# Optimization experiments

Measured on AMD Instinct MI355X. Metric: run time of the kernel, lower is better.

Reference implementation:

```python
import jax, jax.numpy as jnp
import numpy as np

GAMMA = 2
EPS = 1e-8  # torch F.cosine_similarity norm clamp


def setup_inputs() -> dict:
    key = jax.random.key(0)
    k1, k2, k3 = jax.random.split(key, 3)
    b, c, h, w = 32, 256, 32, 32
    x = jax.random.normal(k1, (b, c, h, w), dtype=jnp.float32)
    # 1x1 conv transform_net (num_layers=1): weight (c_out, c_in), bias (c_out,)
    conv_w = jax.random.normal(k2, (c, c), dtype=jnp.float32) / np.sqrt(c)
    conv_b = jax.random.normal(k3, (c,), dtype=jnp.float32) * 0.01
    return {"x": x, "conv_w": conv_w, "conv_b": conv_b}


def reference(x, conv_w, conv_b):
    b, c, h, w = x.shape
    hw = h * w
    xf = x.reshape(b, c, hw)  # (b, c, hw)
    # cosine similarity: normalize channels once, then a single GEMM
    norm = jnp.sqrt(jnp.sum(xf * xf, axis=1, keepdims=True))
    xn = xf / jnp.maximum(norm, EPS)
    sim = jnp.einsum('bcq,bck->bqk', xn, xn)  # (b, hw, hw)
    sim = jax.nn.relu(sim) ** GAMMA
    # 1x1 conv transform
    t = jnp.einsum('oc,bck->bok', conv_w, xf) + conv_b[None, :, None]  # (b, c, hw)
    # weighted aggregation: out[b, c, q] = sum_k sim[b, q, k] * t[b, c, k]
    out = jnp.einsum('bqk,bck->bcq', sim, t)
    return out.reshape(b, c, h, w)
```

## Files before the change

kernel.cpp:

```cpp
#include <hip/hip_runtime.h>
#include <math.h>

#define B 32
#define C 256
#define HW 1024

typedef __attribute__((ext_vector_type(8))) short bf16x8;
typedef __attribute__((ext_vector_type(4))) float f32x4;

__device__ __forceinline__ unsigned short f2bf(float f) {
    unsigned int u = __float_as_uint(f);
    u += 0x7fffu + ((u >> 16) & 1u);
    return (unsigned short)(u >> 16);
}

__device__ __forceinline__ void gload16(const void* g, void* l) {
    __builtin_amdgcn_global_load_lds(
        (const __attribute__((address_space(1))) unsigned int*)g,
        (__attribute__((address_space(3))) unsigned int*)l, 16, 0, 0);
}

__global__ __launch_bounds__(256) void norms_kernel(const float* __restrict__ x,
                                                    float* __restrict__ norm,
                                                    float* __restrict__ rnorm) {
    const int q = blockIdx.x * 256 + threadIdx.x;
    const int b = blockIdx.y;
    const float* xb = x + (size_t)b * C * HW + q;
    float s = 0.f;
#pragma unroll 8
    for (int c = 0; c < C; ++c) {
        float v = xb[(size_t)c * HW];
        s += v * v;
    }
    float n = fmaxf(sqrtf(s), 1e-8f);
    norm[b * HW + q] = n;
    rnorm[b * HW + q] = 1.f / n;
}

__global__ __launch_bounds__(256) void castw_kernel(const float* __restrict__ w,
                                                    unsigned short* __restrict__ wb) {
    int i = (blockIdx.x * 256 + threadIdx.x) * 4;
    float4 v = *(const float4*)(w + i);
    unsigned long long pk = (unsigned long long)f2bf(v.x) |
                            ((unsigned long long)f2bf(v.y) << 16) |
                            ((unsigned long long)f2bf(v.z) << 32) |
                            ((unsigned long long)f2bf(v.w) << 48);
    *(unsigned long long*)(wb + i) = pk;
}

__global__ __launch_bounds__(256) void prep_kernel(const float* __restrict__ x,
                                                   const float* __restrict__ rnorm,
                                                   unsigned short* __restrict__ xnT) {
    __shared__ float tile[64][65];
    const int t = threadIdx.x;
    const int q0 = blockIdx.x * 64, c0 = blockIdx.y * 64, b = blockIdx.z;
    const float* xb = x + ((size_t)b * C + c0) * HW + q0;
#pragma unroll
    for (int p = 0; p < 16; ++p) {
        int cc = p * 4 + (t >> 6);
        int qq = t & 63;
        tile[cc][qq] = xb[(size_t)cc * HW + qq];
    }
    __syncthreads();
    const float* rb = rnorm + b * HW + q0;
#pragma unroll
    for (int p = 0; p < 16; ++p) {
        int qq = p * 4 + (t >> 6);
        int cc = t & 63;
        float v = tile[cc][qq];
        float rn = rb[qq];
        xnT[((size_t)b * HW + q0 + qq) * C + c0 + cc] = f2bf(v * rn);
    }
}

__global__ __launch_bounds__(256) void tgemm_kernel(
    const unsigned short* __restrict__ A,
    const unsigned short* __restrict__ Bm,
    unsigned short* __restrict__ Cb,
    const float* __restrict__ bias, const float* __restrict__ norm) {
    __shared__ unsigned short Asub[128 * 64];
    __shared__ unsigned short Bsub[128 * 64];
    const int t = threadIdx.x;
    const int bz = blockIdx.z;
    const int m0 = blockIdx.y * 128, n0 = blockIdx.x * 128;

    const int ug = ((t & 7) ^ ((t >> 3) & 7)) * 16;
    const char* gA = (const char*)A + (size_t)(m0 + (t >> 3)) * (C * 2) + ug;
    const char* gB = (const char*)(Bm + (size_t)bz * HW * C) +
                     (size_t)(n0 + (t >> 3)) * (C * 2) + ug;
    char* lA = (char*)Asub + t * 16;
    char* lB = (char*)Bsub + t * 16;
    const int rowStep = 32 * C * 2;

    const int lane = t & 63;
    const int wid = t >> 6;
    const int wr = wid >> 1, wc = wid & 1;
    const int lr = lane & 15, hi = lane >> 4;
    int rowA[4], rowB[4], sb[2];
#pragma unroll
    for (int i = 0; i < 4; ++i) rowA[i] = (wr * 64 + i * 16 + lr) * 128;
#pragma unroll
    for (int j = 0; j < 4; ++j) rowB[j] = (wc * 64 + j * 16 + lr) * 128;
#pragma unroll
    for (int kk = 0; kk < 2; ++kk) sb[kk] = ((hi + 4 * kk) ^ (lr & 7)) * 16;

    f32x4 acc[4][4];
#pragma unroll
    for (int i = 0; i < 4; ++i)
#pragma unroll
        for (int j = 0; j < 4; ++j) acc[i][j] = (f32x4)(0.f);

#pragma unroll
    for (int p = 0; p < 4; ++p) {
        gload16(gA + p * rowStep, lA + p * 4096);
        gload16(gB + p * rowStep, lB + p * 4096);
    }
    for (int ks = 0; ks < 4; ++ks) {
        __syncthreads();
#pragma unroll
        for (int kk = 0; kk < 2; ++kk) {
            bf16x8 av[4], bv[4];
#pragma unroll
            for (int i = 0; i < 4; ++i)
                av[i] = *(const bf16x8*)((const char*)Asub + rowA[i] + sb[kk]);
#pragma unroll
            for (int j = 0; j < 4; ++j)
                bv[j] = *(const bf16x8*)((const char*)Bsub + rowB[j] + sb[kk]);
#pragma unroll
            for (int i = 0; i < 4; ++i)
#pragma unroll
                for (int j = 0; j < 4; ++j)
                    acc[i][j] = __builtin_amdgcn_mfma_f32_16x16x32_bf16(
                        av[i], bv[j], acc[i][j], 0, 0, 0);
        }
        __syncthreads();
        if (ks + 1 < 4) {
            const char* gA2 = gA + (size_t)(ks + 1) * 128;
            const char* gB2 = gB + (size_t)(ks + 1) * 128;
#pragma unroll
            for (int p = 0; p < 4; ++p) {
                gload16(gA2 + p * rowStep, lA + p * 4096);
                gload16(gB2 + p * rowStep, lB + p * 4096);
            }
        }
    }
    const int mb = m0 + wr * 64 + hi * 4;
    const int nb = n0 + wc * 64 + lr;
    unsigned short* Cp = Cb + (size_t)bz * C * HW;
    float nrm[4];
#pragma unroll
    for (int j = 0; j < 4; ++j) nrm[j] = norm[bz * HW + nb + j * 16];
#pragma unroll
    for (int i = 0; i < 4; ++i)
#pragma unroll
        for (int r = 0; r < 4; ++r) {
            int m = mb + i * 16 + r;
            float bbv = bias[m];
#pragma unroll
            for (int j = 0; j < 4; ++j)
                Cp[(size_t)m * HW + nb + j * 16] = f2bf(acc[i][j][r] * nrm[j] + bbv);
        }
}

__global__ __launch_bounds__(512, 2) void fused_kernel(
    const unsigned short* __restrict__ xnT,
    const unsigned short* __restrict__ tb,
    float* __restrict__ out) {
    __shared__ unsigned short XQ[128 * 256];
    __shared__ unsigned short XK[128 * 64];
    __shared__ unsigned short SS[128 * 128];
    __shared__ unsigned short TT[256 * 64];
    const int t = threadIdx.x;
    const int b = blockIdx.y;
    const int qg0 = blockIdx.x * 128;
    const int lane = t & 63;
    const int wid = t >> 6;
    const int lr = lane & 15, hi = lane >> 4;

    const char* xq_g = (const char*)(xnT + ((size_t)b * HW + qg0) * C);
    const char* xk_gb = (const char*)(xnT + (size_t)b * HW * C);
    const char* t_gb = (const char*)(tb + (size_t)b * C * HW);

#pragma unroll
    for (int p = 0; p < 8; ++p) {
        int u = p * 512 + t;
        int q = u >> 5, s = u & 31;
        int sp = (s & 16) | ((s & 15) ^ (q & 15));
        gload16(xq_g + (size_t)q * 512 + sp * 16, (char*)XQ + (size_t)u * 16);
    }

    const int qa = wid >> 1, ka = wid & 1;
    const int cb4 = wid >> 1, qb = wid & 1;

    f32x4 oacc[4][4];
#pragma unroll
    for (int i = 0; i < 4; ++i)
#pragma unroll
        for (int j = 0; j < 4; ++j) oacc[i][j] = (f32x4)(0.f);

    for (int kt = 0; kt < 8; ++kt) {
        const int kg0 = kt * 128;
        f32x4 sacc[4][2];
#pragma unroll
        for (int i = 0; i < 4; ++i)
#pragma unroll
            for (int j = 0; j < 2; ++j) sacc[i][j] = (f32x4)(0.f);

        for (int cch = 0; cch < 4; ++cch) {
            __syncthreads();
#pragma unroll
            for (int p = 0; p < 2; ++p) {
                int u = p * 512 + t;
                int k = u >> 3, s = u & 7;
                int sp = s ^ (k & 7);
                gload16(xk_gb + (size_t)(kg0 + k) * 512 + cch * 128 + sp * 16,
                        (char*)XK + (size_t)u * 16);
            }
            if (cch == 0) {
#pragma unroll
                for (int p = 0; p < 4; ++p) {
                    int u = p * 512 + t;
                    int c = u >> 3, s = u & 7;
                    int sp = s ^ (c & 7);
                    gload16(t_gb + (size_t)c * 2048 + kg0 * 2 + sp * 16,
                            (char*)TT + (size_t)u * 16);
                }
            }
            __syncthreads();
#pragma unroll
            for (int cs = 0; cs < 2; ++cs) {
                bf16x8 av[4], bv[2];
#pragma unroll
                for (int i = 0; i < 4; ++i) {
                    int krow = ka * 64 + i * 16 + lr;
                    int off = (cs * 64 + hi * 16) ^ ((krow & 7) << 4);
                    av[i] = *(const bf16x8*)((const char*)XK + krow * 128 + off);
                }
#pragma unroll
                for (int j = 0; j < 2; ++j) {
                    int qrow = qa * 32 + j * 16 + lr;
                    int off = ((cch * 64 + cs * 32) * 2 + hi * 16) ^ ((qrow & 15) << 4);
                    bv[j] = *(const bf16x8*)((const char*)XQ + qrow * 512 + off);
                }
#pragma unroll
                for (int i = 0; i < 4; ++i)
#pragma unroll
                    for (int j = 0; j < 2; ++j)
                        sacc[i][j] = __builtin_amdgcn_mfma_f32_16x16x32_bf16(
                            av[i], bv[j], sacc[i][j], 0, 0, 0);
            }
        }

#pragma unroll
        for (int i = 0; i < 4; ++i)
#pragma unroll
            for (int j = 0; j < 2; ++j) {
                int q = qa * 32 + j * 16 + lr;
                int kb = ka * 64 + i * 16 + hi * 4;
                unsigned long long pk = 0;
#pragma unroll
                for (int r = 0; r < 4; ++r) {
                    float v = fmaxf(sacc[i][j][r], 0.f);
                    v = v * v;
                    pk |= (unsigned long long)f2bf(v) << (16 * r);
                }
                int off = (kb * 2) ^ ((q & 15) << 4);
                *(unsigned long long*)((char*)SS + q * 256 + off) = pk;
            }
        __syncthreads();

#pragma unroll
        for (int tch = 0; tch < 2; ++tch) {
            if (tch == 1) {
                __syncthreads();
#pragma unroll
                for (int p = 0; p < 4; ++p) {
                    int u = p * 512 + t;
                    int c = u >> 3, s = u & 7;
                    int sp = s ^ (c & 7);
                    gload16(t_gb + (size_t)c * 2048 + kg0 * 2 + 128 + sp * 16,
                            (char*)TT + (size_t)u * 16);
                }
                __syncthreads();
            }
#pragma unroll
            for (int ks = 0; ks < 2; ++ks) {
                bf16x8 av[4], bv[4];
#pragma unroll
                for (int i = 0; i < 4; ++i) {
                    int crow = cb4 * 64 + i * 16 + lr;
                    int off = (ks * 64 + hi * 16) ^ ((crow & 7) << 4);
                    av[i] = *(const bf16x8*)((const char*)TT + crow * 128 + off);
                }
#pragma unroll
                for (int j = 0; j < 4; ++j) {
                    int qrow = qb * 64 + j * 16 + lr;
                    int off = (tch * 128 + ks * 64 + hi * 16) ^ ((qrow & 15) << 4);
                    bv[j] = *(const bf16x8*)((const char*)SS + qrow * 256 + off);
                }
#pragma unroll
                for (int i = 0; i < 4; ++i)
#pragma unroll
                    for (int j = 0; j < 4; ++j)
                        oacc[i][j] = __builtin_amdgcn_mfma_f32_16x16x32_bf16(
                            av[i], bv[j], oacc[i][j], 0, 0, 0);
            }
        }
    }

#pragma unroll
    for (int i = 0; i < 4; ++i)
#pragma unroll
        for (int r = 0; r < 4; ++r) {
            int c = cb4 * 64 + i * 16 + hi * 4 + r;
            float* op = out + ((size_t)b * C + c) * HW + qg0 + qb * 64 + lr;
#pragma unroll
            for (int j = 0; j < 4; ++j) op[j * 16] = oacc[i][j][r];
        }
}

extern "C" void kernel_launch(void* const* d_in, const int* in_sizes, int n_in,
                              void* d_out, int out_size, void* d_ws, size_t ws_size,
                              hipStream_t stream) {
    const float* x    = (const float*)d_in[0];
    const float* w    = (const float*)d_in[1];
    const float* bias = (const float*)d_in[2];
    float* out = (float*)d_out;

    char* ws = (char*)d_ws;
    float* norm         = (float*)ws;
    float* rnorm        = (float*)(ws + (128 << 10));
    unsigned short* wbf = (unsigned short*)(ws + (256 << 10));
    unsigned short* xnT = (unsigned short*)(ws + (384 << 10));
    unsigned short* tb  = (unsigned short*)(ws + (384 << 10) + (16u << 20));

    hipLaunchKernelGGL(norms_kernel, dim3(HW / 256, B), dim3(256), 0, stream,
                       x, norm, rnorm);
    hipLaunchKernelGGL(castw_kernel, dim3(C * C / 1024), dim3(256), 0, stream, w, wbf);
    hipLaunchKernelGGL(prep_kernel, dim3(HW / 64, C / 64, B), dim3(256), 0, stream,
                       x, rnorm, xnT);
    hipLaunchKernelGGL(tgemm_kernel, dim3(HW / 128, C / 128, B), dim3(256), 0, stream,
                       wbf, xnT, tb, bias, norm);
    hipLaunchKernelGGL(fused_kernel, dim3(HW / 128, B), dim3(512), 0, stream,
                       xnT, tb, out);
}
```

Measured before the change: 95.48 us.

## Double-buffer XK staging and load T operand directly into registers

The fused kernel now double-buffers the key-side xnT chunks across two LDS buffers with explicit vmcnt waits and raw barriers, so the next chunk's global-to-LDS load overlaps the current MFMA work. The T operand is no longer staged through LDS; each wave loads its T fragments straight from global memory into registers while the similarity GEMM runs. This frees LDS, may allow higher occupancy, and removes several full __syncthreads per tile. In exchange it adds register pressure from the held T fragments, uses uncoalesced direct global loads, and relies on hand-counted vmcnt values that must match the compiler's emitted load order.

```diff
diff --git a/kernel.cpp b/kernel.cpp
--- a/kernel.cpp
+++ b/kernel.cpp
@@ -74,10 +74,9 @@
 }
 
 __global__ __launch_bounds__(256) void tgemm_kernel(
-    const unsigned short* __restrict__ A,
-    const unsigned short* __restrict__ Bm,
-    unsigned short* __restrict__ Cb,
-    const float* __restrict__ bias, const float* __restrict__ norm) {
+    const unsigned short* __restrict__ A, const unsigned short* __restrict__ Bm,
+    unsigned short* __restrict__ Cb, const float* __restrict__ bias,
+    const float* __restrict__ norm) {
     __shared__ unsigned short Asub[128 * 64];
     __shared__ unsigned short Bsub[128 * 64];
     const int t = threadIdx.x;
@@ -167,9 +166,9 @@
     const unsigned short* __restrict__ tb,
     float* __restrict__ out) {
     __shared__ unsigned short XQ[128 * 256];
-    __shared__ unsigned short XK[128 * 64];
+    __shared__ unsigned short XK0[128 * 64];
+    __shared__ unsigned short XK1[128 * 64];
     __shared__ unsigned short SS[128 * 128];
-    __shared__ unsigned short TT[256 * 64];
     const int t = threadIdx.x;
     const int b = blockIdx.y;
     const int qg0 = blockIdx.x * 128;
@@ -181,6 +180,26 @@
     const char* xk_gb = (const char*)(xnT + (size_t)b * HW * C);
     const char* t_gb = (const char*)(tb + (size_t)b * C * HW);
 
+    const int qa = wid >> 1, ka = wid & 1;
+    const int cb4 = wid >> 1, qb = wid & 1;
+
+    auto stage_xk = [&](int kg0, int cch, char* dst) {
+#pragma unroll
+        for (int p = 0; p < 2; ++p) {
+            int u = p * 512 + t;
+            int k = u >> 3, s = u & 7;
+            int sp = s ^ (k & 7);
+            gload16(xk_gb + (size_t)(kg0 + k) * 512 + cch * 128 + sp * 16,
+                    dst + u * 16);
+        }
+    };
+
+    f32x4 oacc[4][4];
+#pragma unroll
+    for (int i = 0; i < 4; ++i)
+#pragma unroll
+        for (int j = 0; j < 4; ++j) oacc[i][j] = (f32x4)(0.f);
+
 #pragma unroll
     for (int p = 0; p < 8; ++p) {
         int u = p * 512 + t;
@@ -188,15 +207,9 @@
         int sp = (s & 16) | ((s & 15) ^ (q & 15));
         gload16(xq_g + (size_t)q * 512 + sp * 16, (char*)XQ + (size_t)u * 16);
     }
-
-    const int qa = wid >> 1, ka = wid & 1;
-    const int cb4 = wid >> 1, qb = wid & 1;
-
-    f32x4 oacc[4][4];
-#pragma unroll
-    for (int i = 0; i < 4; ++i)
-#pragma unroll
-        for (int j = 0; j < 4; ++j) oacc[i][j] = (f32x4)(0.f);
+    stage_xk(0, 0, (char*)XK0);
+    asm volatile("s_waitcnt vmcnt(0)" ::: "memory");
+    __builtin_amdgcn_s_barrier();
 
     for (int kt = 0; kt < 8; ++kt) {
         const int kg0 = kt * 128;
@@ -206,27 +219,7 @@
 #pragma unroll
             for (int j = 0; j < 2; ++j) sacc[i][j] = (f32x4)(0.f);
 
-        for (int cch = 0; cch < 4; ++cch) {
-            __syncthreads();
-#pragma unroll
-            for (int p = 0; p < 2; ++p) {
-                int u = p * 512 + t;
-                int k = u >> 3, s = u & 7;
-                int sp = s ^ (k & 7);
-                gload16(xk_gb + (size_t)(kg0 + k) * 512 + cch * 128 + sp * 16,
-                        (char*)XK + (size_t)u * 16);
-            }
-            if (cch == 0) {
-#pragma unroll
-                for (int p = 0; p < 4; ++p) {
-                    int u = p * 512 + t;
-                    int c = u >> 3, s = u & 7;
-                    int sp = s ^ (c & 7);
-                    gload16(t_gb + (size_t)c * 2048 + kg0 * 2 + sp * 16,
-                            (char*)TT + (size_t)u * 16);
-                }
-            }
-            __syncthreads();
+        auto computeA = [&](const char* xk, int cch) {
 #pragma unroll
             for (int cs = 0; cs < 2; ++cs) {
                 bf16x8 av[4], bv[2];
@@ -234,7 +227,7 @@
                 for (int i = 0; i < 4; ++i) {
                     int krow = ka * 64 + i * 16 + lr;
                     int off = (cs * 64 + hi * 16) ^ ((krow & 7) << 4);
-                    av[i] = *(const bf16x8*)((const char*)XK + krow * 128 + off);
+                    av[i] = *(const bf16x8*)(xk + krow * 128 + off);
                 }
 #pragma unroll
                 for (int j = 0; j < 2; ++j) {
@@ -249,7 +242,38 @@
                         sacc[i][j] = __builtin_amdgcn_mfma_f32_16x16x32_bf16(
                             av[i], bv[j], sacc[i][j], 0, 0, 0);
             }
-        }
+        };
+
+        bf16x8 tt[4][4];
+
+        stage_xk(kg0, 1, (char*)XK1);
+        asm volatile("s_waitcnt vmcnt(2)" ::: "memory");
+        __builtin_amdgcn_s_barrier();
+        computeA((const char*)XK0, 0);
+        __builtin_amdgcn_s_barrier();
+
+        stage_xk(kg0, 2, (char*)XK0);
+        asm volatile("s_waitcnt vmcnt(2)" ::: "memory");
+        __builtin_amdgcn_s_barrier();
+        computeA((const char*)XK1, 1);
+#pragma unroll
+        for (int i = 0; i < 4; ++i)
+#pragma unroll
+            for (int kc = 0; kc < 4; ++kc)
+                tt[i][kc] = *(const bf16x8*)(
+                    t_gb + (size_t)(cb4 * 64 + i * 16 + lr) * 2048 +
+                    (kg0 + kc * 32 + hi * 8) * 2);
+        __builtin_amdgcn_s_barrier();
+
+        stage_xk(kg0, 3, (char*)XK1);
+        asm volatile("s_waitcnt vmcnt(18)" ::: "memory");
+        __builtin_amdgcn_s_barrier();
+        computeA((const char*)XK0, 2);
+        __builtin_amdgcn_s_barrier();
+
+        asm volatile("s_waitcnt vmcnt(0)" ::: "memory");
+        __builtin_amdgcn_s_barrier();
+        computeA((const char*)XK1, 3);
 
 #pragma unroll
         for (int i = 0; i < 4; ++i)
@@ -267,45 +291,28 @@
                 int off = (kb * 2) ^ ((q & 15) << 4);
                 *(unsigned long long*)((char*)SS + q * 256 + off) = pk;
             }
-        __syncthreads();
-
-#pragma unroll
-        for (int tch = 0; tch < 2; ++tch) {
-            if (tch == 1) {
-                __syncthreads();
-#pragma unroll
-                for (int p = 0; p < 4; ++p) {
-                    int u = p * 512 + t;
-                    int c = u >> 3, s = u & 7;
-                    int sp = s ^ (c & 7);
-                    gload16(t_gb + (size_t)c * 2048 + kg0 * 2 + 128 + sp * 16,
-                            (char*)TT + (size_t)u * 16);
-                }
-                __syncthreads();
+        asm volatile("s_waitcnt lgkmcnt(0)" ::: "memory");
+        __builtin_amdgcn_sched_barrier(0);
+        __builtin_amdgcn_s_barrier();
+
+#pragma unroll
+        for (int kc = 0; kc < 4; ++kc) {
+            bf16x8 bv[4];
+#pragma unroll
+            for (int j = 0; j < 4; ++j) {
+                int qrow = qb * 64 + j * 16 + lr;
+                int off = (kc * 64 + hi * 16) ^ ((qrow & 15) << 4);
+                bv[j] = *(const bf16x8*)((const char*)SS + qrow * 256 + off);
             }
 #pragma unroll
-            for (int ks = 0; ks < 2; ++ks) {
-                bf16x8 av[4], bv[4];
-#pragma unroll
-                for (int i = 0; i < 4; ++i) {
-                    int crow = cb4 * 64 + i * 16 + lr;
-                    int off = (ks * 64 + hi * 16) ^ ((crow & 7) << 4);
-                    av[i] = *(const bf16x8*)((const char*)TT + crow * 128 + off);
-                }
-#pragma unroll
-                for (int j = 0; j < 4; ++j) {
-                    int qrow = qb * 64 + j * 16 + lr;
-                    int off = (tch * 128 + ks * 64 + hi * 16) ^ ((qrow & 15) << 4);
-                    bv[j] = *(const bf16x8*)((const char*)SS + qrow * 256 + off);
-                }
-#pragma unroll
-                for (int i = 0; i < 4; ++i)
-#pragma unroll
-                    for (int j = 0; j < 4; ++j)
-                        oacc[i][j] = __builtin_amdgcn_mfma_f32_16x16x32_bf16(
-                            av[i], bv[j], oacc[i][j], 0, 0, 0);
-            }
-        }
+            for (int i = 0; i < 4; ++i)
+#pragma unroll
+                for (int j = 0; j < 4; ++j)
+                    oacc[i][j] = __builtin_amdgcn_mfma_f32_16x16x32_bf16(
+                        tt[i][kc], bv[j], oacc[i][j], 0, 0, 0);
+        }
+
+        if (kt < 7) stage_xk(kg0 + 128, 0, (char*)XK0);
     }
 
 #pragma unroll
```

Measured after the change: 104.5 us. 9.5% more time.

## Fuse norm and transpose prep, shrink fused tile to 64 queries with XCD mapping

Applied to the files above, without the earlier changes.

Merges the norm kernel and the normalize/transpose kernel into one kernel that reads x once per 64-query tile, dropping the rnorm buffer and a launch. The fused similarity/aggregation kernel now handles 64 queries per block instead of 128, using less LDS so four blocks fit per CU and twice as many blocks are launched. Blocks are remapped so that blocks on the same XCD share a batch, which should improve L2 reuse. The T tile is streamed in four smaller chunks with more barriers, and each block does less work per load of K and T, so global traffic for those goes up.

```diff
diff --git a/kernel.cpp b/kernel.cpp
--- a/kernel.cpp
+++ b/kernel.cpp
@@ -20,21 +20,52 @@
         (__attribute__((address_space(3))) unsigned int*)l, 16, 0, 0);
 }
 
-__global__ __launch_bounds__(256) void norms_kernel(const float* __restrict__ x,
+__global__ __launch_bounds__(256) void prepn_kernel(const float* __restrict__ x,
                                                     float* __restrict__ norm,
-                                                    float* __restrict__ rnorm) {
-    const int q = blockIdx.x * 256 + threadIdx.x;
-    const int b = blockIdx.y;
-    const float* xb = x + (size_t)b * C * HW + q;
-    float s = 0.f;
-#pragma unroll 8
-    for (int c = 0; c < C; ++c) {
-        float v = xb[(size_t)c * HW];
-        s += v * v;
-    }
-    float n = fmaxf(sqrtf(s), 1e-8f);
-    norm[b * HW + q] = n;
-    rnorm[b * HW + q] = 1.f / n;
+                                                    unsigned short* __restrict__ xnT) {
+    __shared__ float xt[256][65];
+    __shared__ float psum[4][64];
+    __shared__ float rn[64];
+    const int t = threadIdx.x;
+    const int q0 = blockIdx.x * 64, b = blockIdx.y;
+    const float* xb = x + (size_t)b * C * HW + q0;
+#pragma unroll
+    for (int p = 0; p < 16; ++p) {
+        int u = p * 256 + t;
+        int c = u >> 4, q4 = (u & 15) * 4;
+        float4 v = *(const float4*)(xb + (size_t)c * HW + q4);
+        xt[c][q4] = v.x; xt[c][q4 + 1] = v.y; xt[c][q4 + 2] = v.z; xt[c][q4 + 3] = v.w;
+    }
+    __syncthreads();
+    {
+        int cb = t >> 6, q = t & 63;
+        float s = 0.f;
+#pragma unroll
+        for (int cc = 0; cc < 64; ++cc) {
+            float v = xt[cb * 64 + cc][q];
+            s += v * v;
+        }
+        psum[cb][q] = s;
+    }
+    __syncthreads();
+    if (t < 64) {
+        float s = psum[0][t] + psum[1][t] + psum[2][t] + psum[3][t];
+        float n = fmaxf(sqrtf(s), 1e-8f);
+        norm[b * HW + q0 + t] = n;
+        rn[t] = 1.f / n;
+    }
+    __syncthreads();
+    unsigned short* xrow = xnT + ((size_t)b * HW + q0) * C;
+#pragma unroll
+    for (int p = 0; p < 16; ++p) {
+        int q = p * 4 + (t >> 6);
+        float rnq = rn[q];
+#pragma unroll
+        for (int i = 0; i < 4; ++i) {
+            int c = (t & 63) + 64 * i;
+            xrow[(size_t)q * C + c] = f2bf(xt[c][q] * rnq);
+        }
+    }
 }
 
 __global__ __launch_bounds__(256) void castw_kernel(const float* __restrict__ w,
@@ -48,36 +79,10 @@
     *(unsigned long long*)(wb + i) = pk;
 }
 
-__global__ __launch_bounds__(256) void prep_kernel(const float* __restrict__ x,
-                                                   const float* __restrict__ rnorm,
-                                                   unsigned short* __restrict__ xnT) {
-    __shared__ float tile[64][65];
-    const int t = threadIdx.x;
-    const int q0 = blockIdx.x * 64, c0 = blockIdx.y * 64, b = blockIdx.z;
-    const float* xb = x + ((size_t)b * C + c0) * HW + q0;
-#pragma unroll
-    for (int p = 0; p < 16; ++p) {
-        int cc = p * 4 + (t >> 6);
-        int qq = t & 63;
-        tile[cc][qq] = xb[(size_t)cc * HW + qq];
-    }
-    __syncthreads();
-    const float* rb = rnorm + b * HW + q0;
-#pragma unroll
-    for (int p = 0; p < 16; ++p) {
-        int qq = p * 4 + (t >> 6);
-        int cc = t & 63;
-        float v = tile[cc][qq];
-        float rn = rb[qq];
-        xnT[((size_t)b * HW + q0 + qq) * C + c0 + cc] = f2bf(v * rn);
-    }
-}
-
 __global__ __launch_bounds__(256) void tgemm_kernel(
-    const unsigned short* __restrict__ A,
-    const unsigned short* __restrict__ Bm,
-    unsigned short* __restrict__ Cb,
-    const float* __restrict__ bias, const float* __restrict__ norm) {
+    const unsigned short* __restrict__ A, const unsigned short* __restrict__ Bm,
+    unsigned short* __restrict__ Cb, const float* __restrict__ bias,
+    const float* __restrict__ norm) {
     __shared__ unsigned short Asub[128 * 64];
     __shared__ unsigned short Bsub[128 * 64];
     const int t = threadIdx.x;
@@ -162,47 +167,50 @@
         }
 }
 
-__global__ __launch_bounds__(512, 2) void fused_kernel(
+__global__ __launch_bounds__(512, 4) void fused_kernel(
     const unsigned short* __restrict__ xnT,
     const unsigned short* __restrict__ tb,
     float* __restrict__ out) {
-    __shared__ unsigned short XQ[128 * 256];
+    __shared__ unsigned short XQ[64 * 256];
     __shared__ unsigned short XK[128 * 64];
-    __shared__ unsigned short SS[128 * 128];
-    __shared__ unsigned short TT[256 * 64];
+    __shared__ unsigned short SS[64 * 128];
+    __shared__ unsigned short TT[256 * 32];
     const int t = threadIdx.x;
-    const int b = blockIdx.y;
-    const int qg0 = blockIdx.x * 128;
+    const int wgid = blockIdx.x;
+    const int xcd = wgid & 7, g = wgid >> 3;
+    const int qt = g & 15, bh = g >> 4;
+    const int b = bh * 8 + xcd;
+    const int qg0 = qt * 64;
+
     const int lane = t & 63;
     const int wid = t >> 6;
     const int lr = lane & 15, hi = lane >> 4;
+    const int qh = wid & 1, kq = wid >> 1;
+    const int cq = wid >> 1;
 
     const char* xq_g = (const char*)(xnT + ((size_t)b * HW + qg0) * C);
     const char* xk_gb = (const char*)(xnT + (size_t)b * HW * C);
     const char* t_gb = (const char*)(tb + (size_t)b * C * HW);
 
 #pragma unroll
-    for (int p = 0; p < 8; ++p) {
+    for (int p = 0; p < 4; ++p) {
         int u = p * 512 + t;
         int q = u >> 5, s = u & 31;
         int sp = (s & 16) | ((s & 15) ^ (q & 15));
         gload16(xq_g + (size_t)q * 512 + sp * 16, (char*)XQ + (size_t)u * 16);
     }
 
-    const int qa = wid >> 1, ka = wid & 1;
-    const int cb4 = wid >> 1, qb = wid & 1;
-
-    f32x4 oacc[4][4];
+    f32x4 oacc[4][2];
 #pragma unroll
     for (int i = 0; i < 4; ++i)
 #pragma unroll
-        for (int j = 0; j < 4; ++j) oacc[i][j] = (f32x4)(0.f);
+        for (int j = 0; j < 2; ++j) oacc[i][j] = (f32x4)(0.f);
 
     for (int kt = 0; kt < 8; ++kt) {
         const int kg0 = kt * 128;
-        f32x4 sacc[4][2];
-#pragma unroll
-        for (int i = 0; i < 4; ++i)
+        f32x4 sacc[2][2];
+#pragma unroll
+        for (int i = 0; i < 2; ++i)
 #pragma unroll
             for (int j = 0; j < 2; ++j) sacc[i][j] = (f32x4)(0.f);
 
@@ -216,34 +224,33 @@
                 gload16(xk_gb + (size_t)(kg0 + k) * 512 + cch * 128 + sp * 16,
                         (char*)XK + (size_t)u * 16);
             }
-            if (cch == 0) {
-#pragma unroll
-                for (int p = 0; p < 4; ++p) {
+            if (cch == 3) {
+#pragma unroll
+                for (int p = 0; p < 2; ++p) {
                     int u = p * 512 + t;
-                    int c = u >> 3, s = u & 7;
-                    int sp = s ^ (c & 7);
-                    gload16(t_gb + (size_t)c * 2048 + kg0 * 2 + sp * 16,
+                    int c = u >> 2, s = u & 3;
+                    gload16(t_gb + (size_t)c * 2048 + kg0 * 2 + s * 16,
                             (char*)TT + (size_t)u * 16);
                 }
             }
             __syncthreads();
 #pragma unroll
             for (int cs = 0; cs < 2; ++cs) {
-                bf16x8 av[4], bv[2];
-#pragma unroll
-                for (int i = 0; i < 4; ++i) {
-                    int krow = ka * 64 + i * 16 + lr;
+                bf16x8 av[2], bv[2];
+#pragma unroll
+                for (int i = 0; i < 2; ++i) {
+                    int krow = kq * 32 + i * 16 + lr;
                     int off = (cs * 64 + hi * 16) ^ ((krow & 7) << 4);
                     av[i] = *(const bf16x8*)((const char*)XK + krow * 128 + off);
                 }
 #pragma unroll
                 for (int j = 0; j < 2; ++j) {
-                    int qrow = qa * 32 + j * 16 + lr;
-                    int off = ((cch * 64 + cs * 32) * 2 + hi * 16) ^ ((qrow & 15) << 4);
+                    int qrow = qh * 32 + j * 16 + lr;
+                    int off = (cch * 128 + cs * 64 + hi * 16) ^ ((qrow & 15) << 4);
                     bv[j] = *(const bf16x8*)((const char*)XQ + qrow * 512 + off);
                 }
 #pragma unroll
-                for (int i = 0; i < 4; ++i)
+                for (int i = 0; i < 2; ++i)
 #pragma unroll
                     for (int j = 0; j < 2; ++j)
                         sacc[i][j] = __builtin_amdgcn_mfma_f32_16x16x32_bf16(
@@ -252,11 +259,11 @@
         }
 
 #pragma unroll
-        for (int i = 0; i < 4; ++i)
+        for (int i = 0; i < 2; ++i)
 #pragma unroll
             for (int j = 0; j < 2; ++j) {
-                int q = qa * 32 + j * 16 + lr;
-                int kb = ka * 64 + i * 16 + hi * 4;
+                int q = qh * 32 + j * 16 + lr;
+                int kb = kq * 32 + i * 16 + hi * 4;
                 unsigned long long pk = 0;
 #pragma unroll
                 for (int r = 0; r < 4; ++r) {
@@ -270,41 +277,36 @@
         __syncthreads();
 
 #pragma unroll
-        for (int tch = 0; tch < 2; ++tch) {
-            if (tch == 1) {
+        for (int kc = 0; kc < 4; ++kc) {
+            if (kc > 0) {
                 __syncthreads();
 #pragma unroll
-                for (int p = 0; p < 4; ++p) {
+                for (int p = 0; p < 2; ++p) {
                     int u = p * 512 + t;
-                    int c = u >> 3, s = u & 7;
-                    int sp = s ^ (c & 7);
-                    gload16(t_gb + (size_t)c * 2048 + kg0 * 2 + 128 + sp * 16,
+                    int c = u >> 2, s = u & 3;
+                    gload16(t_gb + (size_t)c * 2048 + (kg0 + kc * 32) * 2 + s * 16,
                             (char*)TT + (size_t)u * 16);
                 }
                 __syncthreads();
             }
-#pragma unroll
-            for (int ks = 0; ks < 2; ++ks) {
-                bf16x8 av[4], bv[4];
-#pragma unroll
-                for (int i = 0; i < 4; ++i) {
-                    int crow = cb4 * 64 + i * 16 + lr;
-                    int off = (ks * 64 + hi * 16) ^ ((crow & 7) << 4);
-                    av[i] = *(const bf16x8*)((const char*)TT + crow * 128 + off);
-                }
-#pragma unroll
-                for (int j = 0; j < 4; ++j) {
-                    int qrow = qb * 64 + j * 16 + lr;
-                    int off = (tch * 128 + ks * 64 + hi * 16) ^ ((qrow & 15) << 4);
-                    bv[j] = *(const bf16x8*)((const char*)SS + qrow * 256 + off);
-                }
-#pragma unroll
-                for (int i = 0; i < 4; ++i)
-#pragma unroll
-                    for (int j = 0; j < 4; ++j)
-                        oacc[i][j] = __builtin_amdgcn_mfma_f32_16x16x32_bf16(
-                            av[i], bv[j], oacc[i][j], 0, 0, 0);
-            }
+            bf16x8 av[4], bv[2];
+#pragma unroll
+            for (int i = 0; i < 4; ++i) {
+                int crow = cq * 64 + i * 16 + lr;
+                av[i] = *(const bf16x8*)((const char*)TT + crow * 64 + hi * 16);
+            }
+#pragma unroll
+            for (int j = 0; j < 2; ++j) {
+                int qrow = qh * 32 + j * 16 + lr;
+                int off = (kc * 64 + hi * 16) ^ ((qrow & 15) << 4);
+                bv[j] = *(const bf16x8*)((const char*)SS + qrow * 256 + off);
+            }
+#pragma unroll
+            for (int i = 0; i < 4; ++i)
+#pragma unroll
+                for (int j = 0; j < 2; ++j)
+                    oacc[i][j] = __builtin_amdgcn_mfma_f32_16x16x32_bf16(
+                        av[i], bv[j], oacc[i][j], 0, 0, 0);
         }
     }
 
@@ -312,10 +314,10 @@
     for (int i = 0; i < 4; ++i)
 #pragma unroll
         for (int r = 0; r < 4; ++r) {
-            int c = cb4 * 64 + i * 16 + hi * 4 + r;
-            float* op = out + ((size_t)b * C + c) * HW + qg0 + qb * 64 + lr;
-#pragma unroll
-            for (int j = 0; j < 4; ++j) op[j * 16] = oacc[i][j][r];
+            int c = cq * 64 + i * 16 + hi * 4 + r;
+            float* op = out + ((size_t)b * C + c) * HW + qg0 + qh * 32 + lr;
+#pragma unroll
+            for (int j = 0; j < 2; ++j) op[j * 16] = oacc[i][j][r];
         }
 }
 
@@ -329,18 +331,15 @@
 
     char* ws = (char*)d_ws;
     float* norm         = (float*)ws;
-    float* rnorm        = (float*)(ws + (128 << 10));
-    unsigned short* wbf = (unsigned short*)(ws + (256 << 10));
-    unsigned short* xnT = (unsigned short*)(ws + (384 << 10));
-    unsigned short* tb  = (unsigned short*)(ws + (384 << 10) + (16u << 20));
-
-    hipLaunchKernelGGL(norms_kernel, dim3(HW / 256, B), dim3(256), 0, stream,
-                       x, norm, rnorm);
+    unsigned short* wbf = (unsigned short*)(ws + (128 << 10));
+    unsigned short* xnT = (unsigned short*)(ws + (256 << 10));
+    unsigned short* tb  = (unsigned short*)(ws + (256 << 10) + (16u << 20));
+
+    hipLaunchKernelGGL(prepn_kernel, dim3(HW / 64, B), dim3(256), 0, stream,
+                       x, norm, xnT);
     hipLaunchKernelGGL(castw_kernel, dim3(C * C / 1024), dim3(256), 0, stream, w, wbf);
-    hipLaunchKernelGGL(prep_kernel, dim3(HW / 64, C / 64, B), dim3(256), 0, stream,
-                       x, rnorm, xnT);
     hipLaunchKernelGGL(tgemm_kernel, dim3(HW / 128, C / 128, B), dim3(256), 0, stream,
                        wbf, xnT, tb, bias, norm);
-    hipLaunchKernelGGL(fused_kernel, dim3(HW / 128, B), dim3(512), 0, stream,
+    hipLaunchKernelGGL(fused_kernel, dim3((HW / 64) * B), dim3(512), 0, stream,
                        xnT, tb, out);
 }
```

Result: faster. 76.74 us (-19.6%).
